# Kernel optimization log

Hardware: AMD Instinct MI355X
Metric: run time of the kernel (lower is better)

Reference implementation:

```python
import jax, jax.numpy as jnp
import numpy as np

B, CIN, L, H, D, A = 2, 512, 1024, 32, 64, 2048  # A = H*D = att_features
SCALE = 0.05


def setup_inputs() -> dict:
    key = jax.random.key(0)
    ks = jax.random.split(key, 11)
    x = jax.random.normal(ks[0], (B, CIN, L), jnp.float32)
    # Per-head 1x1 Conv1d projections stacked over heads: weight [H, D, CIN], bias [H, D]
    Wq = jax.random.normal(ks[1], (H, D, CIN), jnp.float32) * SCALE
    bq = jax.random.normal(ks[2], (H, D), jnp.float32) * SCALE
    Wk = jax.random.normal(ks[3], (H, D, CIN), jnp.float32) * SCALE
    bk = jax.random.normal(ks[4], (H, D), jnp.float32) * SCALE
    Wv = jax.random.normal(ks[5], (H, D, CIN), jnp.float32) * SCALE
    bv = jax.random.normal(ks[6], (H, D), jnp.float32) * SCALE
    # final_block: Conv1d(A,A,1) -> ReLU -> Conv1d(A,A,1)
    W1 = jax.random.normal(ks[7], (A, A), jnp.float32) * SCALE
    b1 = jax.random.normal(ks[8], (A,), jnp.float32) * SCALE
    W2 = jax.random.normal(ks[9], (A, A), jnp.float32) * SCALE
    b2 = jax.random.normal(ks[10], (A,), jnp.float32) * SCALE
    return {"x": x, "Wq": Wq, "bq": bq, "Wk": Wk, "bk": bk,
            "Wv": Wv, "bv": bv, "W1": W1, "b1": b1, "W2": W2, "b2": b2}


def reference(x, Wq, bq, Wk, bk, Wv, bv, W1, b1, W2, b2):
    # 1x1 conv projections for all heads at once: [B,H,D,L]
    q = jnp.einsum('hdc,bcl->bhdl', Wq, x) + bq[None, :, :, None]
    k = jnp.einsum('hdc,bcl->bhdl', Wk, x) + bk[None, :, :, None]
    v = jnp.einsum('hdc,bcl->bhdl', Wv, x) + bv[None, :, :, None]
    # att = bmm(q^T, k): att[b,h,l,m] = sum_d q[b,h,d,l] * k[b,h,d,m]
    att = jnp.einsum('bhdl,bhdm->bhlm', q, k)
    # relative distance bias s_rel[i,j] = -|i-j|
    idx = jnp.arange(L)
    s_rel = -jnp.abs(idx[:, None] - idx[None, :]).astype(x.dtype)  # [L,L]
    att_map = jax.nn.softmax((att + s_rel) / float(np.sqrt(D)), axis=-1)
    # post-softmax upper-triangular mask (torch.triu keeps i <= j)
    masked = jnp.triu(att_map)
    # bmm(value, masked_att): out[b,h,d,m] = sum_l v[b,h,d,l] * masked[b,h,l,m]
    o = jnp.einsum('bhdl,bhlm->bhdm', v, masked)
    # per-head ReLU then concat heads along channel dim -> [B, A, L]
    h = jax.nn.relu(o).reshape(B, H * D, L)
    # final_block: 1x1 conv -> ReLU -> 1x1 conv
    z = jax.nn.relu(jnp.einsum('oc,bcl->bol', W1, h) + b1[None, :, None])
    z = jnp.einsum('oc,bcl->bol', W2, z) + b2[None, :, None]
    return z
```

## Files before the change

kernel.cpp:

```cpp
#include <hip/hip_runtime.h>

#define L 1024
#define CIN 512
#define NH 32
#define DH 64
#define NB 2
#define AF 2048

typedef unsigned short u16;
typedef unsigned int u32;
typedef __attribute__((ext_vector_type(8))) short bfx8;
typedef __attribute__((ext_vector_type(4))) short bfx4;
typedef __attribute__((ext_vector_type(4))) float fx4;

struct __align__(8) us4 { u16 x, y, z, w; };

#define MFMA16 __builtin_amdgcn_mfma_f32_16x16x32_bf16
#define SBAR() __builtin_amdgcn_s_barrier()
#define SFENCE() __builtin_amdgcn_sched_barrier(0)
#define WAIT_VM(N) asm volatile("s_waitcnt vmcnt(" #N ")" ::: "memory")
#define WAIT_LGKM0() asm volatile("s_waitcnt lgkmcnt(0)" ::: "memory")

__device__ inline void gld16(const void* g, void* l) {
    __builtin_amdgcn_global_load_lds(
        (const __attribute__((address_space(1))) u32*)g,
        (__attribute__((address_space(3))) u32*)l, 16, 0, 0);
}

__device__ inline u16 f2b(float f) {
    union { float f; u32 u; } v; v.f = f;
    u32 u = v.u;
    return (u16)((u + 0x7fffu + ((u >> 16) & 1u)) >> 16);
}

__global__ __launch_bounds__(256) void prep(
    const float* __restrict__ x,
    const float* __restrict__ Wq, const float* __restrict__ Wk, const float* __restrict__ Wv,
    const float* __restrict__ W1, const float* __restrict__ W2,
    u16* __restrict__ xT, u16* __restrict__ Wqb, u16* __restrict__ Wkb,
    u16* __restrict__ Wvb, u16* __restrict__ W1b, u16* __restrict__ W2b)
{
    __shared__ u16 tile[64][68];
    const int z = blockIdx.z;
    const int t = threadIdx.x;
    if (z < 5) {
        const float* in; u16* out; int n4;
        switch (z) {
            case 0: in = Wq; out = Wqb; n4 = AF * CIN / 4; break;
            case 1: in = Wk; out = Wkb; n4 = AF * CIN / 4; break;
            case 2: in = Wv; out = Wvb; n4 = AF * CIN / 4; break;
            case 3: in = W1; out = W1b; n4 = AF * AF / 4; break;
            default: in = W2; out = W2b; n4 = AF * AF / 4; break;
        }
        int i = blockIdx.x * 256 + t;
        for (; i < n4; i += 512 * 256) {
            float4 v = ((const float4*)in)[i];
            us4 o = { f2b(v.x), f2b(v.y), f2b(v.z), f2b(v.w) };
            ((us4*)out)[i] = o;
        }
    } else {
        const int bid = blockIdx.x;
        if (bid >= 256) return;
        const int c0 = (bid & 7) * 64, l0 = ((bid >> 3) & 15) * 64, b = bid >> 7;
        const int tr = t >> 4, tc4 = (t & 15) * 4;
        #pragma unroll
        for (int p = 0; p < 4; ++p) {
            int c = p * 16 + tr;
            float4 v = *(const float4*)(x + ((size_t)(b * CIN + c0 + c)) * L + l0 + tc4);
            tile[c][tc4 + 0] = f2b(v.x); tile[c][tc4 + 1] = f2b(v.y);
            tile[c][tc4 + 2] = f2b(v.z); tile[c][tc4 + 3] = f2b(v.w);
        }
        __syncthreads();
        #pragma unroll
        for (int p = 0; p < 4; ++p) {
            int l = p * 16 + tr;
            us4 o = { tile[tc4 + 0][l], tile[tc4 + 1][l], tile[tc4 + 2][l], tile[tc4 + 3][l] };
            *(us4*)(xT + ((size_t)(b * L + l0 + l)) * CIN + c0 + tc4) = o;
        }
    }
}

template<int RELU, int CT_OUT, int NA>
__global__ __launch_bounds__(256) void gemm_bt(
    const u16* __restrict__ A0, const u16* __restrict__ A1, const u16* __restrict__ A2,
    const float* __restrict__ bias0, const float* __restrict__ bias1, const float* __restrict__ bias2,
    const u16* __restrict__ BTb, void* __restrict__ Cb, void* __restrict__ Cb2,
    int M, int N, int K, size_t sBT, size_t sC, size_t sWhich)
{
    const int z = blockIdx.z;
    const int which = (NA == 3) ? (z % 3) : 0;
    const int b     = (NA == 3) ? (z / 3) : z;
    const u16* __restrict__ A = (which == 0) ? A0 : (which == 1) ? A1 : A2;
    const float* __restrict__ bias = (which == 0) ? bias0 : (which == 1) ? bias1 : bias2;
    const u16* __restrict__ BT = BTb + (size_t)b * sBT;

    const int lin  = blockIdx.x + (blockIdx.y << 4);
    const int lin2 = ((lin & 7) << 5) + (lin >> 3);
    const int n0 = (lin2 >> 4) * 64;
    const int m0 = (lin2 & 15) * 128;

    __shared__ u16 lA[6][128 * 32];
    __shared__ u16 lB[6][64 * 32];

    const int t = threadIdx.x, lane = t & 63, wave = t >> 6;
    const int wm = (wave >> 1) * 64, wn = (wave & 1) * 32;
    const int rl = lane & 15, kh = lane >> 4;

    fx4 acc[4][2];
    #pragma unroll
    for (int i = 0; i < 4; ++i)
        #pragma unroll
        for (int j = 0; j < 2; ++j) acc[i][j] = (fx4){0.f, 0.f, 0.f, 0.f};

    const int sA0 = t, sA1 = t + 256, sB = t;
    const int rA0 = sA0 >> 2, cA0 = (sA0 & 3) ^ ((rA0 >> 1) & 3);
    const int rA1 = sA1 >> 2, cA1 = (sA1 & 3) ^ ((rA1 >> 1) & 3);
    const int rB  = sB  >> 2, cB  = (sB  & 3) ^ ((rB  >> 1) & 3);
    const u16* gA0 = A  + (size_t)(m0 + rA0) * K + cA0 * 8;
    const u16* gA1 = A  + (size_t)(m0 + rA1) * K + cA1 * 8;
    const u16* gB0 = BT + (size_t)(n0 + rB) * K + cB * 8;

    int aoff[4], boff[2];
    #pragma unroll
    for (int f = 0; f < 4; ++f) {
        int ra = wm + f * 16 + rl;
        aoff[f] = ra * 32 + ((kh ^ ((ra >> 1) & 3)) * 8);
    }
    #pragma unroll
    for (int f = 0; f < 2; ++f) {
        int rb = wn + f * 16 + rl;
        boff[f] = rb * 32 + ((kh ^ ((rb >> 1) & 3)) * 8);
    }

#define STAGE(BF, K0) do { \
        gld16(gA0 + (K0), &lA[BF][sA0 * 8]); \
        gld16(gA1 + (K0), &lA[BF][sA1 * 8]); \
        gld16(gB0 + (K0), &lB[BF][sB  * 8]); } while (0)

    const int NT = K >> 5;
    STAGE(0, 0); STAGE(1, 32); STAGE(2, 64);
    WAIT_VM(6); SBAR(); SFENCE();

    int bcur = 0, bpre = 3;
    for (int it = 0; it < NT; ++it) {
        if (it + 3 < NT) {
            STAGE(bpre, (it + 3) << 5);
            WAIT_VM(9);
        } else if (it + 2 < NT) {
            WAIT_VM(6);
        } else if (it + 1 < NT) {
            WAIT_VM(3);
        } else {
            WAIT_VM(0);
        }
        SBAR(); SFENCE();
        const u16* bA = lA[bcur];
        const u16* bB = lB[bcur];
        bfx8 af[4], bfr[2];
        #pragma unroll
        for (int f = 0; f < 4; ++f) af[f] = *(const bfx8*)&bA[aoff[f]];
        #pragma unroll
        for (int f = 0; f < 2; ++f) bfr[f] = *(const bfx8*)&bB[boff[f]];
        __builtin_amdgcn_s_setprio(1);
        #pragma unroll
        for (int fm = 0; fm < 4; ++fm)
            #pragma unroll
            for (int fn = 0; fn < 2; ++fn)
                acc[fm][fn] = MFMA16(af[fm], bfr[fn], acc[fm][fn], 0, 0, 0);
        __builtin_amdgcn_s_setprio(0);
        if (++bcur == 6) bcur = 0;
        if (++bpre == 6) bpre = 0;
    }
#undef STAGE

    if (NA == 3 && which == 2) {
        u16* Vn = (u16*)Cb2 + (size_t)b * (size_t)M * N;
        #pragma unroll
        for (int fm = 0; fm < 4; ++fm) {
            int mg = m0 + wm + fm * 16 + kh * 4;
            #pragma unroll
            for (int fn = 0; fn < 2; ++fn) {
                int ng = n0 + wn + fn * 16 + rl;
                #pragma unroll
                for (int r = 0; r < 4; ++r)
                    Vn[(size_t)(mg + r) * N + ng] = f2b(acc[fm][fn][r] + bias[mg + r]);
            }
        }
    } else if (CT_OUT) {
        const float sc = (NA == 3 && which == 0) ? 0.125f : 1.0f;
        u16* CT = (u16*)Cb + (size_t)which * sWhich + (size_t)b * sC;
        #pragma unroll
        for (int fm = 0; fm < 4; ++fm) {
            int mg = m0 + wm + fm * 16 + kh * 4;
            float bi0 = bias[mg], bi1 = bias[mg + 1], bi2 = bias[mg + 2], bi3 = bias[mg + 3];
            #pragma unroll
            for (int fn = 0; fn < 2; ++fn) {
                int ng = n0 + wn + fn * 16 + rl;
                float v0 = (acc[fm][fn][0] + bi0) * sc;
                float v1 = (acc[fm][fn][1] + bi1) * sc;
                float v2 = (acc[fm][fn][2] + bi2) * sc;
                float v3 = (acc[fm][fn][3] + bi3) * sc;
                if (RELU) {
                    v0 = fmaxf(v0, 0.f); v1 = fmaxf(v1, 0.f);
                    v2 = fmaxf(v2, 0.f); v3 = fmaxf(v3, 0.f);
                }
                us4 o = { f2b(v0), f2b(v1), f2b(v2), f2b(v3) };
                *(us4*)(CT + (size_t)ng * M + mg) = o;
            }
        }
    } else {
        float* C = (float*)Cb + (size_t)b * sC;
        #pragma unroll
        for (int fm = 0; fm < 4; ++fm) {
            int mg = m0 + wm + fm * 16 + kh * 4;
            #pragma unroll
            for (int fn = 0; fn < 2; ++fn) {
                int ng = n0 + wn + fn * 16 + rl;
                #pragma unroll
                for (int r = 0; r < 4; ++r) {
                    float v = acc[fm][fn][r] + bias[mg + r];
                    if (RELU) v = fmaxf(v, 0.f);
                    C[(size_t)(mg + r) * N + ng] = v;
                }
            }
        }
    }
}

__global__ __launch_bounds__(256) void attn_stats(
    const u16* __restrict__ qT, const u16* __restrict__ kT,
    float* __restrict__ rinv)
{
    const int lt = blockIdx.x;
    const int bh = blockIdx.y;
    const int b = bh >> 5, h = bh & 31;
    const size_t base = (size_t)b * L * AF + h * DH;

    const int mlo = lt < 2 ? 0 : lt - 2;
    const int mhi = lt > 13 ? 15 : lt + 2;
    const int NTW = mhi - mlo + 1;

    __shared__ u16 lq[64 * 64];
    __shared__ u16 lk[4][64 * 64];
    __shared__ float sS[4][64];

    const int t = threadIdx.x, lane = t & 63, wave = t >> 6;
    const int rl = lane & 15, g = lane >> 4;

    const int s0 = t, s1 = t + 256;
    const int r0 = s0 >> 3, cs0 = (s0 & 7) ^ (r0 & 7);
    const int r1 = s1 >> 3, cs1 = (s1 & 7) ^ (r1 & 7);

    const u16* gk0 = kT + base + (size_t)(mlo * 64 + r0) * AF + cs0 * 8;
    const u16* gk1 = kT + base + (size_t)(mlo * 64 + r1) * AF + cs1 * 8;

    gld16(qT + base + (size_t)(lt * 64 + r0) * AF + cs0 * 8, lq + s0 * 8);
    gld16(qT + base + (size_t)(lt * 64 + r1) * AF + cs1 * 8, lq + s1 * 8);
    gld16(gk0, &lk[0][s0 * 8]);
    gld16(gk1, &lk[0][s1 * 8]);
    gld16(gk0 + (size_t)64 * AF, &lk[1][s0 * 8]);
    gld16(gk1 + (size_t)64 * AF, &lk[1][s1 * 8]);
    WAIT_VM(2); SBAR(); SFENCE();

    const int rmr = wave * 16 + rl;
    const int akoff0 = rmr * 64 + ((g ^ (rmr & 7)) * 8);
    const int akoff1 = rmr * 64 + (((g + 4) ^ (rmr & 7)) * 8);
    bfx8 qf0[4], qf1[4];
    #pragma unroll
    for (int f = 0; f < 4; ++f) {
        int rq = f * 16 + rl;
        qf0[f] = *(const bfx8*)&lq[rq * 64 + ((g ^ (rq & 7)) * 8)];
        qf1[f] = *(const bfx8*)&lq[rq * 64 + (((g + 4) ^ (rq & 7)) * 8)];
    }

    float Sx[4] = {0.f, 0.f, 0.f, 0.f};
    for (int i = 0; i < NTW; ++i) {
        if (i + 2 < NTW) {
            const int bf = (i + 2) & 3;
            gld16(gk0 + (size_t)(i + 2) * 64 * AF, &lk[bf][s0 * 8]);
            gld16(gk1 + (size_t)(i + 2) * 64 * AF, &lk[bf][s1 * 8]);
            WAIT_VM(4);
        } else if (i + 1 < NTW) {
            WAIT_VM(2);
        } else {
            WAIT_VM(0);
        }
        SBAR(); SFENCE();
        const u16* kb = lk[i & 3];
        bfx8 ak0 = *(const bfx8*)&kb[akoff0];
        bfx8 ak1 = *(const bfx8*)&kb[akoff1];
        const float mb = (float)((mlo + i) * 64 + wave * 16 + g * 4);
        #pragma unroll
        for (int fn = 0; fn < 4; ++fn) {
            fx4 att = (fx4){0.f, 0.f, 0.f, 0.f};
            att = MFMA16(ak0, qf0[fn], att, 0, 0, 0);
            att = MFMA16(ak1, qf1[fn], att, 0, 0, 0);
            const float lgf = (float)(lt * 64 + fn * 16 + rl);
            float e0 = __expf(att[0] - 0.125f * fabsf(lgf - mb));
            float e1 = __expf(att[1] - 0.125f * fabsf(lgf - (mb + 1.f)));
            float e2 = __expf(att[2] - 0.125f * fabsf(lgf - (mb + 2.f)));
            float e3 = __expf(att[3] - 0.125f * fabsf(lgf - (mb + 3.f)));
            Sx[fn] += (e0 + e1) + (e2 + e3);
        }
    }
    #pragma unroll
    for (int fn = 0; fn < 4; ++fn) {
        float s_ = Sx[fn];
        s_ += __shfl_xor(s_, 16);
        s_ += __shfl_xor(s_, 32);
        if (lane < 16) sS[wave][fn * 16 + rl] = s_;
    }
    __syncthreads();
    if (t < 64) {
        float s_ = sS[0][t] + sS[1][t] + sS[2][t] + sS[3][t];
        rinv[(size_t)bh * L + lt * 64 + t] = 1.0f / s_;
    }
}

__global__ __launch_bounds__(256) void attn_pv(
    const u16* __restrict__ qT, const u16* __restrict__ kT, const u16* __restrict__ v,
    const float* __restrict__ rinv, u16* __restrict__ hT)
{
    const int mt = blockIdx.x;
    const int bh = blockIdx.y;
    const int b = bh >> 5, h = bh & 31;
    const size_t qkbase = (size_t)b * L * AF + h * DH;
    const size_t vbase  = ((size_t)b * AF + h * DH) * L;
    const size_t rbase  = (size_t)bh * L;

    const int ltlo = mt < 2 ? 0 : mt - 2;
    const int NI = mt - ltlo + 1;
    const int m0 = mt * 64;

    __shared__ u16 lkt[64 * 64];
    __shared__ u16 lqt[2][64 * 64], lv[2][64 * 64];
    __shared__ u16 lw[64 * 68];

    const int t = threadIdx.x, lane = t & 63, wave = t >> 6;
    const int rl = lane & 15, g = lane >> 4;

    const int s0 = t, s1 = t + 256;
    const int r0 = s0 >> 3, cs0 = (s0 & 7) ^ (r0 & 7);
    const int r1 = s1 >> 3, cs1 = (s1 & 7) ^ (r1 & 7);

    const u16* gq0 = qT + qkbase + (size_t)(ltlo * 64 + r0) * AF + cs0 * 8;
    const u16* gq1 = qT + qkbase + (size_t)(ltlo * 64 + r1) * AF + cs1 * 8;
    const u16* gv0 = v + vbase + ltlo * 64 + (size_t)r0 * L + cs0 * 8;
    const u16* gv1 = v + vbase + ltlo * 64 + (size_t)r1 * L + cs1 * 8;

    const int rmr = wave * 16 + rl;
    const int toff0 = rmr * 64 + ((g ^ (rmr & 7)) * 8);
    const int toff1 = rmr * 64 + (((g + 4) ^ (rmr & 7)) * 8);
    int qoff0[4], qoff1[4];
    #pragma unroll
    for (int f = 0; f < 4; ++f) {
        int rq = f * 16 + rl;
        qoff0[f] = rq * 64 + ((g ^ (rq & 7)) * 8);
        qoff1[f] = rq * 64 + (((g + 4) ^ (rq & 7)) * 8);
    }

    gld16(kT + qkbase + (size_t)(m0 + r0) * AF + cs0 * 8, lkt + s0 * 8);
    gld16(kT + qkbase + (size_t)(m0 + r1) * AF + cs1 * 8, lkt + s1 * 8);
    gld16(gq0, &lqt[0][s0 * 8]);
    gld16(gq1, &lqt[0][s1 * 8]);
    gld16(gv0, &lv[0][s0 * 8]);
    gld16(gv1, &lv[0][s1 * 8]);
    WAIT_VM(0); SBAR(); SFENCE();

    fx4 oa[4];
    #pragma unroll
    for (int f = 0; f < 4; ++f) oa[f] = (fx4){0.f, 0.f, 0.f, 0.f};

    int cur = 0;
    for (int i = 0; i < NI; ++i) {
        const int lt = ltlo + i;
        if (i + 1 < NI) {
            gld16(gq0 + (size_t)(i + 1) * 64 * AF, &lqt[cur ^ 1][s0 * 8]);
            gld16(gq1 + (size_t)(i + 1) * 64 * AF, &lqt[cur ^ 1][s1 * 8]);
            gld16(gv0 + (i + 1) * 64, &lv[cur ^ 1][s0 * 8]);
            gld16(gv1 + (i + 1) * 64, &lv[cur ^ 1][s1 * 8]);
        }
        bfx8 ak0 = *(const bfx8*)&lkt[toff0];
        bfx8 ak1 = *(const bfx8*)&lkt[toff1];
        const u16* qb = lqt[cur];
        #pragma unroll
        for (int fn = 0; fn < 4; ++fn) {
            bfx8 q0 = *(const bfx8*)&qb[qoff0[fn]];
            bfx8 q1 = *(const bfx8*)&qb[qoff1[fn]];
            fx4 att = (fx4){0.f, 0.f, 0.f, 0.f};
            att = MFMA16(ak0, q0, att, 0, 0, 0);
            att = MFMA16(ak1, q1, att, 0, 0, 0);
            const int lg = lt * 64 + fn * 16 + rl;
            float ri = rinv[rbase + lg];
            const float db = (float)(lg - (m0 + wave * 16 + g * 4));
            #pragma unroll
            for (int r = 0; r < 4; ++r) {
                int mloc = wave * 16 + g * 4 + r;
                float s = att[r] - 0.125f * fabsf(db - (float)r);
                float w = (lg <= m0 + mloc) ? __expf(s) * ri : 0.f;
                lw[mloc * 68 + fn * 16 + rl] = f2b(w);
            }
        }
        WAIT_LGKM0(); SBAR(); SFENCE();

        const u16* vb = lv[cur];
        bfx8 av0 = *(const bfx8*)&vb[toff0];
        bfx8 av1 = *(const bfx8*)&vb[toff1];
        #pragma unroll
        for (int fn = 0; fn < 4; ++fn) {
            const u16* wrow = &lw[(fn * 16 + rl) * 68];
            union { bfx8 f; bfx4 hh[2]; } w0, w1;
            w0.hh[0] = *(const bfx4*)&wrow[g * 8];
            w0.hh[1] = *(const bfx4*)&wrow[g * 8 + 4];
            w1.hh[0] = *(const bfx4*)&wrow[(g + 4) * 8];
            w1.hh[1] = *(const bfx4*)&wrow[(g + 4) * 8 + 4];
            oa[fn] = MFMA16(av0, w0.f, oa[fn], 0, 0, 0);
            oa[fn] = MFMA16(av1, w1.f, oa[fn], 0, 0, 0);
        }
        WAIT_VM(0); WAIT_LGKM0(); SBAR(); SFENCE();
        cur ^= 1;
    }

    #pragma unroll
    for (int fn = 0; fn < 4; ++fn) {
        int mg = m0 + fn * 16 + rl;
        int cg = h * DH + wave * 16 + g * 4;
        us4 o = { f2b(fmaxf(oa[fn][0], 0.f)), f2b(fmaxf(oa[fn][1], 0.f)),
                  f2b(fmaxf(oa[fn][2], 0.f)), f2b(fmaxf(oa[fn][3], 0.f)) };
        *(us4*)(hT + ((size_t)b * L + mg) * AF + cg) = o;
    }
}

extern "C" void kernel_launch(void* const* d_in, const int* in_sizes, int n_in,
                              void* d_out, int out_size, void* d_ws, size_t ws_size,
                              hipStream_t stream)
{
    (void)in_sizes; (void)n_in; (void)out_size; (void)ws_size;
    const float* x  = (const float*)d_in[0];
    const float* Wq = (const float*)d_in[1];
    const float* bq = (const float*)d_in[2];
    const float* Wk = (const float*)d_in[3];
    const float* bk = (const float*)d_in[4];
    const float* Wv = (const float*)d_in[5];
    const float* bv = (const float*)d_in[6];
    const float* W1 = (const float*)d_in[7];
    const float* b1 = (const float*)d_in[8];
    const float* W2 = (const float*)d_in[9];
    const float* b2 = (const float*)d_in[10];

    u16* wsp = (u16*)d_ws;
    size_t o = 0;
    u16* xT  = wsp + o; o += (size_t)NB * L * CIN;
    u16* qT  = wsp + o; o += (size_t)NB * L * AF;
    u16* kT  = wsp + o; o += (size_t)NB * L * AF;
    u16* vdm = wsp + o; o += (size_t)NB * AF * L;
    u16* hT  = wsp + o; o += (size_t)NB * L * AF;
    u16* z1T = wsp + o; o += (size_t)NB * L * AF;
    u16* Wqb = wsp + o; o += (size_t)AF * CIN;
    u16* Wkb = wsp + o; o += (size_t)AF * CIN;
    u16* Wvb = wsp + o; o += (size_t)AF * CIN;
    u16* W1b = wsp + o; o += (size_t)AF * AF;
    u16* W2b = wsp + o; o += (size_t)AF * AF;
    float* rinv = (float*)(wsp + o); o += (size_t)NB * NH * L * 2;

    dim3 blk(256);

    prep<<<dim3(512, 1, 6), blk, 0, stream>>>(x, Wq, Wk, Wv, W1, W2,
                                              xT, Wqb, Wkb, Wvb, W1b, W2b);

    gemm_bt<0, 1, 3><<<dim3(16, 16, NB * 3), blk, 0, stream>>>(
        Wqb, Wkb, Wvb, bq, bk, bv, xT, qT, vdm,
        AF, L, CIN, (size_t)L * CIN, (size_t)L * AF, (size_t)NB * L * AF);

    attn_stats<<<dim3(16, NB * NH), blk, 0, stream>>>(qT, kT, rinv);
    attn_pv<<<dim3(16, NB * NH), blk, 0, stream>>>(qT, kT, vdm, rinv, hT);

    gemm_bt<1, 1, 1><<<dim3(16, 16, NB), blk, 0, stream>>>(
        W1b, nullptr, nullptr, b1, nullptr, nullptr, hT, z1T, nullptr,
        AF, L, AF, (size_t)L * AF, (size_t)L * AF, 0);
    gemm_bt<0, 0, 1><<<dim3(16, 16, NB), blk, 0, stream>>>(
        W2b, nullptr, nullptr, b2, nullptr, nullptr, z1T, d_out, nullptr,
        AF, L, AF, (size_t)L * AF, (size_t)AF * L, 0);
}
```

Baseline: 146.8 us.

## Enlarge GEMM tiles to 128x128 with 4-stage ring and XCD-aware tile mapping

```diff
diff --git a/kernel.cpp b/kernel.cpp
--- a/kernel.cpp
+++ b/kernel.cpp
@@ -94,82 +94,74 @@
     const float* __restrict__ bias = (which == 0) ? bias0 : (which == 1) ? bias1 : bias2;
     const u16* __restrict__ BT = BTb + (size_t)b * sBT;
 
-    const int lin  = blockIdx.x + (blockIdx.y << 4);
-    const int lin2 = ((lin & 7) << 5) + (lin >> 3);
-    const int n0 = (lin2 >> 4) * 64;
-    const int m0 = (lin2 & 15) * 128;
-
-    __shared__ u16 lA[6][128 * 32];
-    __shared__ u16 lB[6][64 * 32];
+    const int lin = blockIdx.x + (blockIdx.y << 3);
+    const int xcd = lin & 7, idx = lin >> 3;
+    const int m0 = (xcd * 2 + (idx >> 3)) * 128;
+    const int n0 = (idx & 7) * 128;
+
+    __shared__ u16 lA[4][128 * 32];
+    __shared__ u16 lB[4][128 * 32];
 
     const int t = threadIdx.x, lane = t & 63, wave = t >> 6;
-    const int wm = (wave >> 1) * 64, wn = (wave & 1) * 32;
+    const int wm = (wave >> 1) * 64, wn = (wave & 1) * 64;
     const int rl = lane & 15, kh = lane >> 4;
 
-    fx4 acc[4][2];
+    fx4 acc[4][4];
     #pragma unroll
     for (int i = 0; i < 4; ++i)
         #pragma unroll
-        for (int j = 0; j < 2; ++j) acc[i][j] = (fx4){0.f, 0.f, 0.f, 0.f};
-
-    const int sA0 = t, sA1 = t + 256, sB = t;
-    const int rA0 = sA0 >> 2, cA0 = (sA0 & 3) ^ ((rA0 >> 1) & 3);
-    const int rA1 = sA1 >> 2, cA1 = (sA1 & 3) ^ ((rA1 >> 1) & 3);
-    const int rB  = sB  >> 2, cB  = (sB  & 3) ^ ((rB  >> 1) & 3);
-    const u16* gA0 = A  + (size_t)(m0 + rA0) * K + cA0 * 8;
-    const u16* gA1 = A  + (size_t)(m0 + rA1) * K + cA1 * 8;
-    const u16* gB0 = BT + (size_t)(n0 + rB) * K + cB * 8;
-
-    int aoff[4], boff[2];
+        for (int j = 0; j < 4; ++j) acc[i][j] = (fx4){0.f, 0.f, 0.f, 0.f};
+
+    const int s0 = t, s1 = t + 256;
+    const int r0 = s0 >> 2, cs0 = (s0 & 3) ^ ((r0 >> 1) & 3);
+    const int r1 = s1 >> 2, cs1 = (s1 & 3) ^ ((r1 >> 1) & 3);
+    const u16* gA0 = A  + (size_t)(m0 + r0) * K + cs0 * 8;
+    const u16* gA1 = A  + (size_t)(m0 + r1) * K + cs1 * 8;
+    const u16* gB0 = BT + (size_t)(n0 + r0) * K + cs0 * 8;
+    const u16* gB1 = BT + (size_t)(n0 + r1) * K + cs1 * 8;
+
+    int aoff[4], boff[4];
     #pragma unroll
     for (int f = 0; f < 4; ++f) {
         int ra = wm + f * 16 + rl;
+        int rb = wn + f * 16 + rl;
         aoff[f] = ra * 32 + ((kh ^ ((ra >> 1) & 3)) * 8);
-    }
-    #pragma unroll
-    for (int f = 0; f < 2; ++f) {
-        int rb = wn + f * 16 + rl;
         boff[f] = rb * 32 + ((kh ^ ((rb >> 1) & 3)) * 8);
     }
 
 #define STAGE(BF, K0) do { \
-        gld16(gA0 + (K0), &lA[BF][sA0 * 8]); \
-        gld16(gA1 + (K0), &lA[BF][sA1 * 8]); \
-        gld16(gB0 + (K0), &lB[BF][sB  * 8]); } while (0)
+        gld16(gA0 + (K0), &lA[BF][s0 * 8]); \
+        gld16(gA1 + (K0), &lA[BF][s1 * 8]); \
+        gld16(gB0 + (K0), &lB[BF][s0 * 8]); \
+        gld16(gB1 + (K0), &lB[BF][s1 * 8]); } while (0)
 
     const int NT = K >> 5;
     STAGE(0, 0); STAGE(1, 32); STAGE(2, 64);
-    WAIT_VM(6); SBAR(); SFENCE();
-
-    int bcur = 0, bpre = 3;
+
     for (int it = 0; it < NT; ++it) {
-        if (it + 3 < NT) {
-            STAGE(bpre, (it + 3) << 5);
-            WAIT_VM(9);
-        } else if (it + 2 < NT) {
-            WAIT_VM(6);
+        if (it + 2 < NT) {
+            WAIT_VM(8);
         } else if (it + 1 < NT) {
-            WAIT_VM(3);
+            WAIT_VM(4);
         } else {
             WAIT_VM(0);
         }
         SBAR(); SFENCE();
-        const u16* bA = lA[bcur];
-        const u16* bB = lB[bcur];
-        bfx8 af[4], bfr[2];
+        if (it + 3 < NT) STAGE((it + 3) & 3, (it + 3) << 5);
+        const u16* bA = lA[it & 3];
+        const u16* bB = lB[it & 3];
+        bfx8 af[4], bfr[4];
         #pragma unroll
         for (int f = 0; f < 4; ++f) af[f] = *(const bfx8*)&bA[aoff[f]];
         #pragma unroll
-        for (int f = 0; f < 2; ++f) bfr[f] = *(const bfx8*)&bB[boff[f]];
+        for (int f = 0; f < 4; ++f) bfr[f] = *(const bfx8*)&bB[boff[f]];
         __builtin_amdgcn_s_setprio(1);
         #pragma unroll
         for (int fm = 0; fm < 4; ++fm)
             #pragma unroll
-            for (int fn = 0; fn < 2; ++fn)
+            for (int fn = 0; fn < 4; ++fn)
                 acc[fm][fn] = MFMA16(af[fm], bfr[fn], acc[fm][fn], 0, 0, 0);
         __builtin_amdgcn_s_setprio(0);
-        if (++bcur == 6) bcur = 0;
-        if (++bpre == 6) bpre = 0;
     }
 #undef STAGE
 
@@ -179,7 +171,7 @@
         for (int fm = 0; fm < 4; ++fm) {
             int mg = m0 + wm + fm * 16 + kh * 4;
             #pragma unroll
-            for (int fn = 0; fn < 2; ++fn) {
+            for (int fn = 0; fn < 4; ++fn) {
                 int ng = n0 + wn + fn * 16 + rl;
                 #pragma unroll
                 for (int r = 0; r < 4; ++r)
@@ -194,7 +186,7 @@
             int mg = m0 + wm + fm * 16 + kh * 4;
             float bi0 = bias[mg], bi1 = bias[mg + 1], bi2 = bias[mg + 2], bi3 = bias[mg + 3];
             #pragma unroll
-            for (int fn = 0; fn < 2; ++fn) {
+            for (int fn = 0; fn < 4; ++fn) {
                 int ng = n0 + wn + fn * 16 + rl;
                 float v0 = (acc[fm][fn][0] + bi0) * sc;
                 float v1 = (acc[fm][fn][1] + bi1) * sc;
@@ -214,7 +206,7 @@
         for (int fm = 0; fm < 4; ++fm) {
             int mg = m0 + wm + fm * 16 + kh * 4;
             #pragma unroll
-            for (int fn = 0; fn < 2; ++fn) {
+            for (int fn = 0; fn < 4; ++fn) {
                 int ng = n0 + wn + fn * 16 + rl;
                 #pragma unroll
                 for (int r = 0; r < 4; ++r) {
@@ -468,17 +460,17 @@
     prep<<<dim3(512, 1, 6), blk, 0, stream>>>(x, Wq, Wk, Wv, W1, W2,
                                               xT, Wqb, Wkb, Wvb, W1b, W2b);
 
-    gemm_bt<0, 1, 3><<<dim3(16, 16, NB * 3), blk, 0, stream>>>(
+    gemm_bt<0, 1, 3><<<dim3(8, 16, NB * 3), blk, 0, stream>>>(
         Wqb, Wkb, Wvb, bq, bk, bv, xT, qT, vdm,
         AF, L, CIN, (size_t)L * CIN, (size_t)L * AF, (size_t)NB * L * AF);
 
     attn_stats<<<dim3(16, NB * NH), blk, 0, stream>>>(qT, kT, rinv);
     attn_pv<<<dim3(16, NB * NH), blk, 0, stream>>>(qT, kT, vdm, rinv, hT);
 
-    gemm_bt<1, 1, 1><<<dim3(16, 16, NB), blk, 0, stream>>>(
+    gemm_bt<1, 1, 1><<<dim3(8, 16, NB), blk, 0, stream>>>(
         W1b, nullptr, nullptr, b1, nullptr, nullptr, hT, z1T, nullptr,
         AF, L, AF, (size_t)L * AF, (size_t)L * AF, 0);
-    gemm_bt<0, 0, 1><<<dim3(16, 16, NB), blk, 0, stream>>>(
+    gemm_bt<0, 0, 1><<<dim3(8, 16, NB), blk, 0, stream>>>(
         W2b, nullptr, nullptr, b2, nullptr, nullptr, z1T, d_out, nullptr,
         AF, L, AF, (size_t)L * AF, (size_t)AF * L, 0);
 }
```

New measurement: 156.6 us. 6.6% more time.

## Double-buffer LDS fragment reads and deepen global prefetch in GEMM main loop

Applied to the files above, without the earlier changes.

```diff
diff --git a/kernel.cpp b/kernel.cpp
--- a/kernel.cpp
+++ b/kernel.cpp
@@ -137,41 +137,59 @@
         gld16(gA1 + (K0), &lA[BF][sA1 * 8]); \
         gld16(gB0 + (K0), &lB[BF][sB  * 8]); } while (0)
 
+#define RDFRAG(BF, AF, BFr) do { \
+        const u16* bA_ = &lA[BF][0]; \
+        const u16* bB_ = &lB[BF][0]; \
+        AF[0] = *(const bfx8*)&bA_[aoff[0]]; \
+        AF[1] = *(const bfx8*)&bA_[aoff[1]]; \
+        AF[2] = *(const bfx8*)&bA_[aoff[2]]; \
+        AF[3] = *(const bfx8*)&bA_[aoff[3]]; \
+        BFr[0] = *(const bfx8*)&bB_[boff[0]]; \
+        BFr[1] = *(const bfx8*)&bB_[boff[1]]; } while (0)
+
+#define DOMFMA(AF, BFr) do { \
+        __builtin_amdgcn_s_setprio(1); \
+        acc[0][0] = MFMA16(AF[0], BFr[0], acc[0][0], 0, 0, 0); \
+        acc[0][1] = MFMA16(AF[0], BFr[1], acc[0][1], 0, 0, 0); \
+        acc[1][0] = MFMA16(AF[1], BFr[0], acc[1][0], 0, 0, 0); \
+        acc[1][1] = MFMA16(AF[1], BFr[1], acc[1][1], 0, 0, 0); \
+        acc[2][0] = MFMA16(AF[2], BFr[0], acc[2][0], 0, 0, 0); \
+        acc[2][1] = MFMA16(AF[2], BFr[1], acc[2][1], 0, 0, 0); \
+        acc[3][0] = MFMA16(AF[3], BFr[0], acc[3][0], 0, 0, 0); \
+        acc[3][1] = MFMA16(AF[3], BFr[1], acc[3][1], 0, 0, 0); \
+        __builtin_amdgcn_s_setprio(0); } while (0)
+
     const int NT = K >> 5;
-    STAGE(0, 0); STAGE(1, 32); STAGE(2, 64);
+    STAGE(0, 0); STAGE(1, 32); STAGE(2, 64); STAGE(3, 96);
     WAIT_VM(6); SBAR(); SFENCE();
 
-    int bcur = 0, bpre = 3;
-    for (int it = 0; it < NT; ++it) {
-        if (it + 3 < NT) {
-            STAGE(bpre, (it + 3) << 5);
-            WAIT_VM(9);
-        } else if (it + 2 < NT) {
-            WAIT_VM(6);
-        } else if (it + 1 < NT) {
-            WAIT_VM(3);
-        } else {
-            WAIT_VM(0);
-        }
+    bfx8 afA[4], bfA[2], afB[4], bfB[2];
+    RDFRAG(0, afA, bfA);
+
+    for (int it = 0; it < NT; it += 2) {
+        if (it + 4 < NT) STAGE((it + 4) % 6, (it + 4) << 5);
+        RDFRAG((it + 1) % 6, afB, bfB);
+        SFENCE();
+        DOMFMA(afA, bfA);
+        if (it + 4 < NT) { WAIT_VM(6); }
+        else if (it + 3 < NT) { WAIT_VM(3); }
+        else { WAIT_VM(0); }
         SBAR(); SFENCE();
-        const u16* bA = lA[bcur];
-        const u16* bB = lB[bcur];
-        bfx8 af[4], bfr[2];
-        #pragma unroll
-        for (int f = 0; f < 4; ++f) af[f] = *(const bfx8*)&bA[aoff[f]];
-        #pragma unroll
-        for (int f = 0; f < 2; ++f) bfr[f] = *(const bfx8*)&bB[boff[f]];
-        __builtin_amdgcn_s_setprio(1);
-        #pragma unroll
-        for (int fm = 0; fm < 4; ++fm)
-            #pragma unroll
-            for (int fn = 0; fn < 2; ++fn)
-                acc[fm][fn] = MFMA16(af[fm], bfr[fn], acc[fm][fn], 0, 0, 0);
-        __builtin_amdgcn_s_setprio(0);
-        if (++bcur == 6) bcur = 0;
-        if (++bpre == 6) bpre = 0;
+
+        if (it + 5 < NT) STAGE((it + 5) % 6, (it + 5) << 5);
+        if (it + 2 < NT) RDFRAG((it + 2) % 6, afA, bfA);
+        SFENCE();
+        DOMFMA(afB, bfB);
+        if (it + 2 < NT) {
+            if (it + 5 < NT) { WAIT_VM(6); }
+            else if (it + 4 < NT) { WAIT_VM(3); }
+            else { WAIT_VM(0); }
+            SBAR(); SFENCE();
+        }
     }
 #undef STAGE
+#undef RDFRAG
+#undef DOMFMA
 
     if (NA == 3 && which == 2) {
         u16* Vn = (u16*)Cb2 + (size_t)b * (size_t)M * N;
```

New measurement: 171.6 us. 1.17x slower.
